# Kernel tuning notes

Measured on AMD Instinct MI355X. Metric: run time of the kernel, lower is better.

## Reference

```python
import jax, jax.numpy as jnp
import numpy as np

B, TQ, TK, D, NA = 8, 512, 2048, 1024, 512
H, HD = 16, 64          # n_head, head_dim (D = H*HD)
NE, HID = 4, 32         # n_experts, expert hidden_dim
EPS = 1e-6


def _rmsnorm(x, w):
    return x * jax.lax.rsqrt(jnp.mean(x * x, axis=-1, keepdims=True) + EPS) * w


def setup_inputs() -> dict:
    key = jax.random.key(0)
    ks = jax.random.split(key, 20)
    r = lambda i, shp: jax.random.normal(ks[i], shp, dtype=jnp.float32) * 0.02
    return {
        'q': jax.random.normal(ks[0], (B, TQ, D), dtype=jnp.float32),
        'kv': jax.random.normal(ks[1], (B, TK, D), dtype=jnp.float32),
        'qn_w': jnp.ones((D,), jnp.float32),
        'kva_w': jnp.ones((D,), jnp.float32),
        'kvi_w': jnp.ones((D,), jnp.float32),
        'dn_w': jnp.ones((D,), jnp.float32),
        'fn_w': jnp.ones((D,), jnp.float32),
        'Wq': r(2, (D, D)), 'bq': jnp.zeros((D,), jnp.float32),
        'Wk': r(3, (D, D)), 'bk': jnp.zeros((D,), jnp.float32),
        'Wv': r(4, (D, D)), 'bv': jnp.zeros((D,), jnp.float32),
        'Wo': r(5, (D, D)), 'bo': jnp.zeros((D,), jnp.float32),
        'active_bias': r(6, (D,)),
        'inactive_bias': r(7, (D,)),
        'log_temp': jnp.array(0.0, jnp.float32),
        'gate_attn': jnp.array(0.3, jnp.float32),
        'gate_ffn': jnp.array(0.7, jnp.float32),
        'Wr': r(8, (D, NE)), 'br': jnp.zeros((NE,), jnp.float32),
        'W1': r(9, (NE, D, 2 * HID)), 'b1': jnp.zeros((NE, 2 * HID), jnp.float32),
        'W2': r(10, (NE, HID, D)), 'b2': jnp.zeros((NE, D), jnp.float32),
        'kv_mask': jnp.ones((B, TK), bool),
        'n_actives': NA,
    }


def _forward(q, kv, qn_w, kva_w, kvi_w, dn_w, fn_w,
             Wq, bq, Wk, bk, Wv, bv, Wo, bo,
             active_bias, inactive_bias, log_temp, gate_attn, gate_ffn,
             Wr, br, W1, b1, W2, b2, kv_mask, n_actives):
    Na = int(n_actives)
    Tk = kv.shape[1]
    Ni = Tk - Na
    b, tq, d = q.shape

    # split-normed kv, with active/inactive learned biases injected pre-KV-proj
    kv_a = _rmsnorm(kv[:, :Na], kva_w) + active_bias
    kv_i = _rmsnorm(kv[:, Na:], kvi_w) + inactive_bias
    kv_b = jnp.concatenate([kv_a, kv_i], axis=1)

    qn = _rmsnorm(q, qn_w)
    qp = (qn @ Wq + bq).reshape(b, tq, H, HD).transpose(0, 2, 1, 3)  # (B,H,Tq,hd)
    k = (kv_b @ Wk + bk).reshape(b, Tk, H, HD).transpose(0, 2, 1, 3)
    v = (kv_b @ Wv + bv).reshape(b, Tk, H, HD).transpose(0, 2, 1, 3)

    # torch: q *= 1/sqrt(hd), then SDPA(q/temp, ...) applies another 1/sqrt(hd)
    temp = jnp.clip(jnp.exp(log_temp), 0.1, 10.0)
    scale = 1.0 / (HD * temp)

    def attn(kk, vv):
        logits = jnp.einsum('bhqd,bhkd->bhqk', qp, kk) * scale
        return jnp.einsum('bhqk,bhkd->bhqd', jax.nn.softmax(logits, axis=-1), vv)

    out = attn(k[:, :, :Na], v[:, :, :Na]) / np.sqrt(max(Na, 1)) \
        - attn(k[:, :, Na:], v[:, :, Na:]) / np.sqrt(max(Ni, 1))
    out = out.transpose(0, 2, 1, 3).reshape(b, tq, d)
    delta = _rmsnorm(out @ Wo + bo, dn_w)
    q_new = q + jax.nn.sigmoid(gate_attn) * delta

    # dense soft MoE over normed kv, with query-similarity logit bias
    x = _rmsnorm(kv, fn_w)
    logits = x @ Wr + br                                   # (B,Tk,NE)
    q_vec = jnp.mean(q_new, axis=1, keepdims=True)         # (B,1,D)
    sim = jnp.einsum('bqd,btd->bt', q_vec, x)              # (B,Tk)
    probs = jax.nn.softmax(logits + sim[..., None], axis=-1)

    h = jnp.einsum('btd,edh->bteh', x, W1) + b1            # (B,Tk,NE,2*HID)
    xp, g = h[..., :HID], h[..., HID:]
    act = xp * (g * jax.nn.sigmoid(g))                     # SwiGLU
    eo = jnp.einsum('bteh,ehd->bted', act, W2) + b2        # (B,Tk,NE,D)
    moe_out = jnp.einsum('bte,bted->btd', probs, eo)

    kv_new = kv + jax.nn.sigmoid(gate_ffn) * moe_out
    return q_new, kv_new


def reference(q, kv, qn_w, kva_w, kvi_w, dn_w, fn_w,
              Wq, bq, Wk, bk, Wv, bv, Wo, bo,
              active_bias, inactive_bias, log_temp, gate_attn, gate_ffn,
              Wr, br, W1, b1, W2, b2, kv_mask, n_actives):
    return _forward(q, kv, qn_w, kva_w, kvi_w, dn_w, fn_w,
                    Wq, bq, Wk, bk, Wv, bv, Wo, bo,
                    active_bias, inactive_bias, log_temp, gate_attn, gate_ffn,
                    Wr, br, W1, b1, W2, b2, kv_mask, n_actives)
```

## Files before the change

kernel.cpp:

```cpp
#include <hip/hip_runtime.h>
#include <hip/hip_bf16.h>
#include <stdint.h>


#define B_   8
#define TQ_  512
#define TK_  2048
#define D_   1024
#define H_   16
#define HD_  64
#define NE_  4
#define HID_ 32
#define EPSF 1e-6f
#define LOG2E 1.44269504f

typedef __bf16 bf16_t;
typedef __bf16 bf16x8 __attribute__((ext_vector_type(8)));
typedef __bf16 bf16x4 __attribute__((ext_vector_type(4)));
typedef float  f32x4  __attribute__((ext_vector_type(4)));

typedef __attribute__((address_space(1))) void gvoid_t;
typedef __attribute__((address_space(3))) void lvoid_t;

__device__ __forceinline__ void gld_lds16(const void* g, void* l) {
  __builtin_amdgcn_global_load_lds((gvoid_t*)g, (lvoid_t*)l, 16, 0, 0);
}

__global__ void transpose_conv_kernel(const float* __restrict__ in, bf16_t* __restrict__ out,
                                      int R, int C, int in_bstride,
                                      int out_rstride, int ob_row, int ob_col) {
  __shared__ float tile[32][33];
  const int bz = blockIdx.z;
  const int rb = blockIdx.y * 32, cb = blockIdx.x * 32;
  const int txi = threadIdx.x, tyi = threadIdx.y;
  const float* inp = in + (size_t)bz * in_bstride;
#pragma unroll
  for (int i = 0; i < 32; i += 8) {
    const int r = rb + tyi + i, c = cb + txi;
    if (r < R && c < C) tile[tyi + i][txi] = inp[(size_t)r * C + c];
  }
  __syncthreads();
#pragma unroll
  for (int i = 0; i < 32; i += 8) {
    const int orow = cb + tyi + i;
    const int ocol = rb + txi;
    if (orow < C && ocol < R)
      out[(size_t)(orow + bz * ob_row) * out_rstride + bz * ob_col + ocol] =
          (bf16_t)tile[txi][tyi + i];
  }
}

__device__ __forceinline__ float block_rsum(float v, float* red) {
  v += __shfl_xor(v, 1);  v += __shfl_xor(v, 2);  v += __shfl_xor(v, 4);
  v += __shfl_xor(v, 8);  v += __shfl_xor(v, 16); v += __shfl_xor(v, 32);
  const int tid = threadIdx.x;
  if ((tid & 63) == 0) red[tid >> 6] = v;
  __syncthreads();
  return red[0] + red[1] + red[2] + red[3];
}

__global__ __launch_bounds__(256)
void rms_kv_kernel(const float* __restrict__ kv, const float* __restrict__ kva_w,
                   const float* __restrict__ kvi_w, const float* __restrict__ fn_w,
                   const float* __restrict__ ab, const float* __restrict__ ib,
                   const int* __restrict__ n_act, const float* __restrict__ Wr,
                   const float* __restrict__ br,
                   bf16_t* __restrict__ kvb, bf16_t* __restrict__ xn,
                   float* __restrict__ probs) {
  __shared__ float red[4];
  __shared__ f32x4 pred[4];
  const int row = blockIdx.x;
  const int t = row & (TK_ - 1);
  const int tid = threadIdx.x;
  const float* src = kv + (size_t)row * D_;
  f32x4 v = ((const f32x4*)src)[tid];
  float ss = v[0]*v[0] + v[1]*v[1] + v[2]*v[2] + v[3]*v[3];
  ss = block_rsum(ss, red);
  const float rs = rsqrtf(ss * (1.0f / D_) + EPSF);
  const int Na = n_act[0];
  const float* wsel = (t < Na) ? kva_w : kvi_w;
  const float* bsel = (t < Na) ? ab : ib;
  const int d = tid * 4;
  f32x4 wv = *(const f32x4*)(wsel + d);
  f32x4 bv = *(const f32x4*)(bsel + d);
  f32x4 fv = *(const f32x4*)(fn_w + d);
  bf16x4 o0, o1;
  f32x4 p4 = {};
#pragma unroll
  for (int c = 0; c < 4; ++c) {
    const float xv = v[c] * rs;
    const float xf = xv * fv[c];
    o0[c] = (bf16_t)(xv * wv[c] + bv[c]);
    o1[c] = (bf16_t)xf;
    const f32x4 w4 = *(const f32x4*)&Wr[(d + c) * 4];
    p4 += w4 * xf;
  }
  *(bf16x4*)&kvb[(size_t)row * D_ + d] = o0;
  *(bf16x4*)&xn [(size_t)row * D_ + d] = o1;
#pragma unroll
  for (int m = 1; m <= 32; m <<= 1) {
    p4[0] += __shfl_xor(p4[0], m); p4[1] += __shfl_xor(p4[1], m);
    p4[2] += __shfl_xor(p4[2], m); p4[3] += __shfl_xor(p4[3], m);
  }
  if ((tid & 63) == 0) pred[tid >> 6] = p4;
  __syncthreads();
  if (tid == 0) {
    f32x4 s = pred[0] + pred[1] + pred[2] + pred[3];
    s[0] += br[0]; s[1] += br[1]; s[2] += br[2]; s[3] += br[3];
    const float mx = fmaxf(fmaxf(s[0], s[1]), fmaxf(s[2], s[3]));
    const float e0 = __expf(s[0] - mx), e1 = __expf(s[1] - mx);
    const float e2 = __expf(s[2] - mx), e3 = __expf(s[3] - mx);
    const float inv = 1.0f / (e0 + e1 + e2 + e3);
    f32x4 pr = { e0 * inv, e1 * inv, e2 * inv, e3 * inv };
    *(f32x4*)&probs[row * 4] = pr;
  }
}

__global__ __launch_bounds__(256)
void rms_q_kernel(const float* __restrict__ q, const float* __restrict__ qn_w,
                  bf16_t* __restrict__ qn) {
  __shared__ float red[4];
  const int row = blockIdx.x;
  const int tid = threadIdx.x;
  const float* src = q + (size_t)row * D_;
  f32x4 v = ((const f32x4*)src)[tid];
  float ss = v[0]*v[0] + v[1]*v[1] + v[2]*v[2] + v[3]*v[3];
  ss = block_rsum(ss, red);
  const float rs = rsqrtf(ss * (1.0f / D_) + EPSF);
  const int d = tid * 4;
  f32x4 wv = *(const f32x4*)(qn_w + d);
  bf16x4 o0;
#pragma unroll
  for (int c = 0; c < 4; ++c) o0[c] = (bf16_t)(v[c] * rs * wv[c]);
  *(bf16x4*)&qn[(size_t)row * D_ + d] = o0;
}

template<int HAS_BIAS>
__global__ __launch_bounds__(256)
void gemm_tn(const bf16_t* __restrict__ A, const bf16_t* __restrict__ Wt,
             const float* __restrict__ bias, bf16_t* __restrict__ C,
             int M, int N, int K) {
  __shared__ alignas(16) bf16_t As[128 * 32];
  __shared__ alignas(16) bf16_t Bs[128 * 32];
  const int tid = threadIdx.x;
  const int lane = tid & 63;
  const int w = tid >> 6;
  const int wr = w >> 1, wc = w & 1;
  const int m0 = blockIdx.x * 128;
  const int n0 = blockIdx.y * 128;

  f32x4 acc[4][4] = {};

  const int eidx = tid * 8;
  const int srow = eidx >> 5;
  const int scol = eidx & 31;
  const bf16_t* ga = A  + (size_t)(m0 + srow) * K + scol;
  const bf16_t* gb = Wt + (size_t)(n0 + srow) * K + scol;
  bf16_t* la0 = &As[tid * 8];
  bf16_t* la1 = &As[2048 + tid * 8];
  bf16_t* lb0 = &Bs[tid * 8];
  bf16_t* lb1 = &Bs[2048 + tid * 8];
  const size_t rstep = (size_t)64 * K;

  const int kb = (lane >> 4) * 8;
  const int ar  = (wr * 64 + (lane & 15)) * 32 + kb;
  const int br2 = (wc * 64 + (lane & 15)) * 32 + kb;

  for (int k0 = 0; k0 < K; k0 += 32) {
    gld_lds16(ga + k0,         la0);
    gld_lds16(ga + k0 + rstep, la1);
    gld_lds16(gb + k0,         lb0);
    gld_lds16(gb + k0 + rstep, lb1);
    __syncthreads();
    bf16x8 af[4], bfr[4];
#pragma unroll
    for (int i = 0; i < 4; ++i) af[i]  = *(const bf16x8*)&As[ar  + i * 512];
#pragma unroll
    for (int j = 0; j < 4; ++j) bfr[j] = *(const bf16x8*)&Bs[br2 + j * 512];
#pragma unroll
    for (int i = 0; i < 4; ++i)
#pragma unroll
      for (int j = 0; j < 4; ++j)
        acc[i][j] = __builtin_amdgcn_mfma_f32_16x16x32_bf16(af[i], bfr[j], acc[i][j], 0, 0, 0);
    __syncthreads();
  }

  const int row0 = m0 + wr * 64 + ((lane >> 4) << 2);
  const int col0 = n0 + wc * 64 + (lane & 15);
#pragma unroll
  for (int j = 0; j < 4; ++j) {
    const int cc = col0 + j * 16;
    const float bv = HAS_BIAS ? bias[cc] : 0.0f;
#pragma unroll
    for (int i = 0; i < 4; ++i) {
      const int rr = row0 + i * 16;
#pragma unroll
      for (int r = 0; r < 4; ++r)
        C[(size_t)(rr + r) * N + cc] = (bf16_t)(acc[i][j][r] + bv);
    }
  }
}

__global__ __launch_bounds__(256)
void gemm_vt(const bf16_t* __restrict__ A, const bf16_t* __restrict__ Wt0,
             const float* __restrict__ bias, bf16_t* __restrict__ C0) {
  __shared__ alignas(16) bf16_t As[128 * 32];
  __shared__ alignas(16) bf16_t Bs[128 * 32];
  const int K = D_, N = TK_;
  const bf16_t* Wt = Wt0 + (size_t)blockIdx.z * TK_ * D_;
  bf16_t* C = C0 + (size_t)blockIdx.z * D_ * TK_;
  const int tid = threadIdx.x;
  const int lane = tid & 63;
  const int w = tid >> 6;
  const int wr = w >> 1, wc = w & 1;
  const int m0 = blockIdx.x * 128;
  const int n0 = blockIdx.y * 128;

  f32x4 acc[4][4] = {};

  const int eidx = tid * 8;
  const int srow = eidx >> 5;
  const int scol = eidx & 31;
  const bf16_t* ga = A  + (size_t)(m0 + srow) * K + scol;
  const bf16_t* gb = Wt + (size_t)(n0 + srow) * K + scol;
  bf16_t* la0 = &As[tid * 8];
  bf16_t* la1 = &As[2048 + tid * 8];
  bf16_t* lb0 = &Bs[tid * 8];
  bf16_t* lb1 = &Bs[2048 + tid * 8];
  const size_t rstep = (size_t)64 * K;

  const int kb = (lane >> 4) * 8;
  const int ar  = (wr * 64 + (lane & 15)) * 32 + kb;
  const int br2 = (wc * 64 + (lane & 15)) * 32 + kb;

  for (int k0 = 0; k0 < K; k0 += 32) {
    gld_lds16(ga + k0,         la0);
    gld_lds16(ga + k0 + rstep, la1);
    gld_lds16(gb + k0,         lb0);
    gld_lds16(gb + k0 + rstep, lb1);
    __syncthreads();
    bf16x8 af[4], bfr[4];
#pragma unroll
    for (int i = 0; i < 4; ++i) af[i]  = *(const bf16x8*)&As[ar  + i * 512];
#pragma unroll
    for (int j = 0; j < 4; ++j) bfr[j] = *(const bf16x8*)&Bs[br2 + j * 512];
#pragma unroll
    for (int i = 0; i < 4; ++i)
#pragma unroll
      for (int j = 0; j < 4; ++j)
        acc[i][j] = __builtin_amdgcn_mfma_f32_16x16x32_bf16(af[i], bfr[j], acc[i][j], 0, 0, 0);
    __syncthreads();
  }

  const int row0 = m0 + wr * 64 + ((lane >> 4) << 2);
  const int col0 = n0 + wc * 64 + (lane & 15);
#pragma unroll
  for (int i = 0; i < 4; ++i) {
    const int rr = row0 + i * 16;
#pragma unroll
    for (int r = 0; r < 4; ++r) {
      const float bv = bias[rr + r];
#pragma unroll
      for (int j = 0; j < 4; ++j)
        C[(size_t)(rr + r) * N + col0 + j * 16] = (bf16_t)(acc[i][j][r] + bv);
    }
  }
}

__global__ __launch_bounds__(256)
void gemm_h_act(const bf16_t* __restrict__ A, const bf16_t* __restrict__ Wt,
                const float* __restrict__ bias, const float* __restrict__ probs,
                bf16_t* __restrict__ a2) {
  __shared__ alignas(16) bf16_t As[128 * 32];
  __shared__ alignas(16) bf16_t Bs[128 * 32];
  const int K = D_;
  const int tid = threadIdx.x;
  const int lane = tid & 63;
  const int w = tid >> 6;
  const int wr = w >> 1, wc = w & 1;
  const int m0 = blockIdx.x * 128;
  const int n0 = blockIdx.y * 128;

  f32x4 acc[4][4] = {};

  const int eidx = tid * 8;
  const int srow = eidx >> 5;
  const int scol = eidx & 31;
  const bf16_t* ga = A  + (size_t)(m0 + srow) * K + scol;
  const bf16_t* gb = Wt + (size_t)(n0 + srow) * K + scol;
  bf16_t* la0 = &As[tid * 8];
  bf16_t* la1 = &As[2048 + tid * 8];
  bf16_t* lb0 = &Bs[tid * 8];
  bf16_t* lb1 = &Bs[2048 + tid * 8];
  const size_t rstep = (size_t)64 * K;

  const int kb = (lane >> 4) * 8;
  const int ar  = (wr * 64 + (lane & 15)) * 32 + kb;
  const int br2 = (wc * 64 + (lane & 15)) * 32 + kb;

  for (int k0 = 0; k0 < K; k0 += 32) {
    gld_lds16(ga + k0,         la0);
    gld_lds16(ga + k0 + rstep, la1);
    gld_lds16(gb + k0,         lb0);
    gld_lds16(gb + k0 + rstep, lb1);
    __syncthreads();
    bf16x8 af[4], bfr[4];
#pragma unroll
    for (int i = 0; i < 4; ++i) af[i]  = *(const bf16x8*)&As[ar  + i * 512];
#pragma unroll
    for (int j = 0; j < 4; ++j) bfr[j] = *(const bf16x8*)&Bs[br2 + j * 512];
#pragma unroll
    for (int i = 0; i < 4; ++i)
#pragma unroll
      for (int j = 0; j < 4; ++j)
        acc[i][j] = __builtin_amdgcn_mfma_f32_16x16x32_bf16(af[i], bfr[j], acc[i][j], 0, 0, 0);
    __syncthreads();
  }

  const int row0 = m0 + wr * 64 + ((lane >> 4) << 2);
  const int hbase = n0 + wc * 64 + (lane & 15);
  const int e = hbase >> 6;
#pragma unroll
  for (int j = 0; j < 2; ++j) {
    const int ch = hbase + j * 16;
    const float bx = bias[ch], bg = bias[ch + 32];
    const int ac = (ch & 63) + e * 32;
#pragma unroll
    for (int i = 0; i < 4; ++i) {
      const int rr = row0 + i * 16;
#pragma unroll
      for (int r = 0; r < 4; ++r) {
        const float xp = acc[i][j][r] + bx;
        const float g  = acc[i][j + 2][r] + bg;
        const float sg = 1.0f / (1.0f + __expf(-g));
        const float pr = probs[(size_t)(rr + r) * 4 + e];
        a2[(size_t)(rr + r) * 128 + ac] = (bf16_t)(pr * xp * g * sg);
      }
    }
  }
}

__global__ __launch_bounds__(256)
void gemm_moe_kvnew(const bf16_t* __restrict__ A, const bf16_t* __restrict__ Wt,
                    const float* __restrict__ kv, const float* __restrict__ probs,
                    const float* __restrict__ b2, const float* __restrict__ gate_ffn,
                    float* __restrict__ out) {
  __shared__ alignas(16) bf16_t As[128 * 32];
  __shared__ alignas(16) bf16_t Bs[128 * 32];
  const int K = 128, N = D_;
  const int tid = threadIdx.x;
  const int lane = tid & 63;
  const int w = tid >> 6;
  const int wr = w >> 1, wc = w & 1;
  const int m0 = blockIdx.x * 128;
  const int n0 = blockIdx.y * 128;

  f32x4 acc[4][4] = {};

  const int eidx = tid * 8;
  const int srow = eidx >> 5;
  const int scol = eidx & 31;
  const bf16_t* ga = A  + (size_t)(m0 + srow) * K + scol;
  const bf16_t* gb = Wt + (size_t)(n0 + srow) * K + scol;
  bf16_t* la0 = &As[tid * 8];
  bf16_t* la1 = &As[2048 + tid * 8];
  bf16_t* lb0 = &Bs[tid * 8];
  bf16_t* lb1 = &Bs[2048 + tid * 8];
  const size_t rstep = (size_t)64 * K;

  const int kb = (lane >> 4) * 8;
  const int ar  = (wr * 64 + (lane & 15)) * 32 + kb;
  const int br2 = (wc * 64 + (lane & 15)) * 32 + kb;

  for (int k0 = 0; k0 < K; k0 += 32) {
    gld_lds16(ga + k0,         la0);
    gld_lds16(ga + k0 + rstep, la1);
    gld_lds16(gb + k0,         lb0);
    gld_lds16(gb + k0 + rstep, lb1);
    __syncthreads();
    bf16x8 af[4], bfr[4];
#pragma unroll
    for (int i = 0; i < 4; ++i) af[i]  = *(const bf16x8*)&As[ar  + i * 512];
#pragma unroll
    for (int j = 0; j < 4; ++j) bfr[j] = *(const bf16x8*)&Bs[br2 + j * 512];
#pragma unroll
    for (int i = 0; i < 4; ++i)
#pragma unroll
      for (int j = 0; j < 4; ++j)
        acc[i][j] = __builtin_amdgcn_mfma_f32_16x16x32_bf16(af[i], bfr[j], acc[i][j], 0, 0, 0);
    __syncthreads();
  }

  const float sgf = 1.0f / (1.0f + __expf(-gate_ffn[0]));
  const int row0 = m0 + wr * 64 + ((lane >> 4) << 2);
  const int col0 = n0 + wc * 64 + (lane & 15);
#pragma unroll
  for (int j = 0; j < 4; ++j) {
    const int cc = col0 + j * 16;
    const f32x4 b2v = { b2[0 * D_ + cc], b2[1 * D_ + cc], b2[2 * D_ + cc], b2[3 * D_ + cc] };
#pragma unroll
    for (int i = 0; i < 4; ++i) {
      const int rr = row0 + i * 16;
#pragma unroll
      for (int r = 0; r < 4; ++r) {
        const f32x4 pr = *(const f32x4*)&probs[(size_t)(rr + r) * 4];
        const float bsum = pr[0]*b2v[0] + pr[1]*b2v[1] + pr[2]*b2v[2] + pr[3]*b2v[3];
        out[(size_t)(rr + r) * N + cc] =
            kv[(size_t)(rr + r) * N + cc] + sgf * (acc[i][j][r] + bsum);
      }
    }
  }
}

__global__ __launch_bounds__(512, 2)
void attn_mfma_kernel(const bf16_t* __restrict__ qp, const bf16_t* __restrict__ kb,
                      const bf16_t* __restrict__ vt, bf16_t* __restrict__ attno,
                      const float* __restrict__ log_temp, const int* __restrict__ n_act) {
  __shared__ alignas(16) bf16_t Ks[2][64 * 64];
  __shared__ alignas(16) bf16_t Vs[2][64 * 64];
  __shared__ alignas(16) bf16_t Ps[8][16 * 64];

  const int dd = blockIdx.x;
  const int xcd = dd & 7, within = dd >> 3;
  const int qt = within & 3, slot = within >> 2;
  const int bh = slot * 8 + xcd;
  const int b = bh >> 4, h = bh & 15;

  const int tid = threadIdx.x;
  const int lane = tid & 63;
  const int w = tid >> 6;
  const int lane15 = lane & 15, lgrp = lane >> 4, l7 = lane & 7;
  const int Na = n_act[0];
  float temp = __expf(log_temp[0]);
  temp = fminf(fmaxf(temp, 0.1f), 10.0f);
  const float lsc = LOG2E / (64.0f * temp);
  const int q0 = qt * 128;

  const bf16_t* qsrc = qp + (size_t)(b * TQ_ + q0 + w * 16 + lane15) * D_ + h * 64 + lgrp * 8;
  const bf16x8 qf0 = *(const bf16x8*)qsrc;
  const bf16x8 qf1 = *(const bf16x8*)(qsrc + 32);

  const int srow = tid >> 3;
  const int schunk = (tid & 7) ^ (srow & 7);
  const bf16_t* ksrc = kb + (size_t)(b * TK_ + srow) * D_ + h * 64 + schunk * 8;
  const bf16_t* vsrc = vt + ((size_t)(b * 16 + h) * 64 + srow) * TK_ + schunk * 8;

  f32x4 o[4] = {};
  f32x4 outa[4] = {};
  f32x4 lacc = {};

  const float inv_sa = rsqrtf((float)(Na > 1 ? Na : 1));
  const int Ni = TK_ - Na;
  const float inv_si = rsqrtf((float)(Ni > 1 ? Ni : 1));

  gld_lds16(ksrc, &Ks[0][tid * 8]);
  gld_lds16(vsrc, &Vs[0][tid * 8]);

  for (int t = 0; t < TK_ / 64; ++t) {
    const int cur = t & 1;
    __syncthreads();
    if (t + 1 < TK_ / 64) {
      const int nb = cur ^ 1;
      gld_lds16(ksrc + (size_t)(t + 1) * 64 * D_, &Ks[nb][tid * 8]);
      gld_lds16(vsrc + (size_t)(t + 1) * 64,      &Vs[nb][tid * 8]);
    }

    f32x4 sacc[4];
#pragma unroll
    for (int cf = 0; cf < 4; ++cf) {
      const int krow = (cf * 16 + lane15) * 64;
      const bf16x8 kf0 = *(const bf16x8*)&Ks[cur][krow + ((lgrp ^ l7) << 3)];
      const bf16x8 kf1 = *(const bf16x8*)&Ks[cur][krow + (((lgrp + 4) ^ l7) << 3)];
      f32x4 s = {};
      s = __builtin_amdgcn_mfma_f32_16x16x32_bf16(qf0, kf0, s, 0, 0, 0);
      s = __builtin_amdgcn_mfma_f32_16x16x32_bf16(qf1, kf1, s, 0, 0, 0);
      sacc[cf] = s;
    }

#pragma unroll
    for (int cf = 0; cf < 4; ++cf) {
      const int kp = cf * 16 + lane15;
      const int kcb = kp >> 3, kin = kp & 7;
      f32x4 p;
#pragma unroll
      for (int r = 0; r < 4; ++r) p[r] = exp2f(sacc[cf][r] * lsc);
      lacc += p;
#pragma unroll
      for (int r = 0; r < 4; ++r) {
        const int ql = lgrp * 4 + r;
        Ps[w][ql * 64 + ((kcb ^ (ql & 7)) << 3) + kin] = (bf16_t)p[r];
      }
    }

    {
      const int prow = lane15 * 64;
      const bf16x8 pa0 = *(const bf16x8*)&Ps[w][prow + ((lgrp ^ l7) << 3)];
      const bf16x8 pa1 = *(const bf16x8*)&Ps[w][prow + (((lgrp + 4) ^ l7) << 3)];
#pragma unroll
      for (int df = 0; df < 4; ++df) {
        const int vrow = (df * 16 + lane15) * 64;
        const bf16x8 vf0 = *(const bf16x8*)&Vs[cur][vrow + ((lgrp ^ l7) << 3)];
        const bf16x8 vf1 = *(const bf16x8*)&Vs[cur][vrow + (((lgrp + 4) ^ l7) << 3)];
        o[df] = __builtin_amdgcn_mfma_f32_16x16x32_bf16(pa0, vf0, o[df], 0, 0, 0);
        o[df] = __builtin_amdgcn_mfma_f32_16x16x32_bf16(pa1, vf1, o[df], 0, 0, 0);
      }
    }

    const bool endA = ((t + 1) * 64 == Na);
    const bool endI = (t == TK_ / 64 - 1);
    if (endA || endI) {
      const float ssc = endA ? inv_sa : -inv_si;
      f32x4 rl = lacc;
#pragma unroll
      for (int r = 0; r < 4; ++r) {
        rl[r] += __shfl_xor(rl[r], 1);
        rl[r] += __shfl_xor(rl[r], 2);
        rl[r] += __shfl_xor(rl[r], 4);
        rl[r] += __shfl_xor(rl[r], 8);
      }
      f32x4 iv;
#pragma unroll
      for (int r = 0; r < 4; ++r) iv[r] = ssc / rl[r];
#pragma unroll
      for (int df = 0; df < 4; ++df) { outa[df] += o[df] * iv; o[df] = (f32x4){}; }
      lacc = (f32x4){};
    }
  }

#pragma unroll
  for (int df = 0; df < 4; ++df)
#pragma unroll
    for (int r = 0; r < 4; ++r)
      attno[(size_t)(b * TQ_ + q0 + w * 16 + lgrp * 4 + r) * D_ + h * 64 + df * 16 + lane15] =
          (bf16_t)outa[df][r];
}

__global__ __launch_bounds__(256)
void delta_qnew_kernel(const bf16_t* __restrict__ proj, const float* __restrict__ dn_w,
                       const float* __restrict__ q, const float* __restrict__ gate_attn,
                       float* __restrict__ qnew) {
  __shared__ float red[4];
  const int row = blockIdx.x;
  const int tid = threadIdx.x;
  bf16x4 pv = *(const bf16x4*)(proj + (size_t)row * D_ + tid * 4);
  f32x4 v;
#pragma unroll
  for (int c = 0; c < 4; ++c) v[c] = (float)pv[c];
  float ss = v[0]*v[0] + v[1]*v[1] + v[2]*v[2] + v[3]*v[3];
  ss = block_rsum(ss, red);
  const float rs = rsqrtf(ss * (1.0f / D_) + EPSF);
  const float sga = 1.0f / (1.0f + __expf(-gate_attn[0]));
  const int d = tid * 4;
  f32x4 wv = *(const f32x4*)(dn_w + d);
  f32x4 qv = *(const f32x4*)(q + (size_t)row * D_ + d);
  f32x4 out;
#pragma unroll
  for (int c = 0; c < 4; ++c) out[c] = qv[c] + sga * (v[c] * rs * wv[c]);
  *(f32x4*)&qnew[(size_t)row * D_ + d] = out;
}

extern "C" void kernel_launch(void* const* d_in, const int* in_sizes, int n_in,
                              void* d_out, int out_size, void* d_ws, size_t ws_size,
                              hipStream_t stream) {
  const float* q           = (const float*)d_in[0];
  const float* kv          = (const float*)d_in[1];
  const float* qn_w        = (const float*)d_in[2];
  const float* kva_w       = (const float*)d_in[3];
  const float* kvi_w       = (const float*)d_in[4];
  const float* dn_w        = (const float*)d_in[5];
  const float* fn_w        = (const float*)d_in[6];
  const float* Wq          = (const float*)d_in[7];
  const float* bq          = (const float*)d_in[8];
  const float* Wk          = (const float*)d_in[9];
  const float* bk          = (const float*)d_in[10];
  const float* Wv          = (const float*)d_in[11];
  const float* bv          = (const float*)d_in[12];
  const float* Wo          = (const float*)d_in[13];
  const float* bo          = (const float*)d_in[14];
  const float* active_bias = (const float*)d_in[15];
  const float* inactive_b  = (const float*)d_in[16];
  const float* log_temp    = (const float*)d_in[17];
  const float* gate_attn   = (const float*)d_in[18];
  const float* gate_ffn    = (const float*)d_in[19];
  const float* Wr          = (const float*)d_in[20];
  const float* br          = (const float*)d_in[21];
  const float* W1          = (const float*)d_in[22];
  const float* b1          = (const float*)d_in[23];
  const float* W2          = (const float*)d_in[24];
  const float* b2          = (const float*)d_in[25];
  const int*   n_act       = (const int*)d_in[27];

  char* ws = (char*)d_ws;
  size_t off = 0;
  auto alloc = [&](size_t bytes) -> char* {
    char* p = ws + off;
    off = (off + bytes + 255) & ~(size_t)255;
    return p;
  };

  bf16_t* wqT  = (bf16_t*)alloc((size_t)D_ * D_ * 2);
  bf16_t* wkT  = (bf16_t*)alloc((size_t)D_ * D_ * 2);
  bf16_t* wvT  = (bf16_t*)alloc((size_t)D_ * D_ * 2);
  bf16_t* woT  = (bf16_t*)alloc((size_t)D_ * D_ * 2);
  bf16_t* w1T  = (bf16_t*)alloc((size_t)256 * D_ * 2);
  bf16_t* w2T  = (bf16_t*)alloc((size_t)D_ * 128 * 2);
  bf16_t* kvb  = (bf16_t*)alloc((size_t)B_ * TK_ * D_ * 2);
  bf16_t* xn   = (bf16_t*)alloc((size_t)B_ * TK_ * D_ * 2);
  bf16_t* qn   = (bf16_t*)alloc((size_t)B_ * TQ_ * D_ * 2);
  bf16_t* qp   = (bf16_t*)alloc((size_t)B_ * TQ_ * D_ * 2);
  bf16_t* kbuf = (bf16_t*)alloc((size_t)B_ * TK_ * D_ * 2);
  bf16_t* vt   = (bf16_t*)alloc((size_t)B_ * D_ * TK_ * 2);
  float*  probs = (float*)alloc((size_t)B_ * TK_ * NE_ * 4);
  bf16_t* attno = qn;
  bf16_t* proj  = qp;
  bf16_t* a2buf = kbuf;
  (void)ws_size; (void)in_sizes; (void)n_in; (void)out_size;

  float* q_new_out  = (float*)d_out;
  float* kv_new_out = (float*)d_out + (size_t)B_ * TQ_ * D_;

  dim3 tb(32, 8);
  transpose_conv_kernel<<<dim3(32, 32, 1), tb, 0, stream>>>(Wq, wqT, D_, D_, 0, D_, 0, 0);
  transpose_conv_kernel<<<dim3(32, 32, 1), tb, 0, stream>>>(Wk, wkT, D_, D_, 0, D_, 0, 0);
  transpose_conv_kernel<<<dim3(32, 32, 1), tb, 0, stream>>>(Wv, wvT, D_, D_, 0, D_, 0, 0);
  transpose_conv_kernel<<<dim3(32, 32, 1), tb, 0, stream>>>(Wo, woT, D_, D_, 0, D_, 0, 0);
  transpose_conv_kernel<<<dim3(2, 32, 4), tb, 0, stream>>>(W1, w1T, D_, 64, D_ * 64, D_, 64, 0);
  transpose_conv_kernel<<<dim3(32, 1, 4), tb, 0, stream>>>(W2, w2T, 32, D_, 32 * D_, 128, 0, 32);

  rms_kv_kernel<<<B_ * TK_, 256, 0, stream>>>(kv, kva_w, kvi_w, fn_w, active_bias,
                                              inactive_b, n_act, Wr, br, kvb, xn, probs);
  rms_q_kernel<<<B_ * TQ_, 256, 0, stream>>>(q, qn_w, qn);

  gemm_tn<1><<<dim3(B_ * TQ_ / 128, D_ / 128), 256, 0, stream>>>(qn, wqT, bq, qp, B_ * TQ_, D_, D_);
  gemm_tn<1><<<dim3(B_ * TK_ / 128, D_ / 128), 256, 0, stream>>>(kvb, wkT, bk, kbuf, B_ * TK_, D_, D_);
  gemm_vt<<<dim3(D_ / 128, TK_ / 128, B_), 256, 0, stream>>>(wvT, kvb, bv, vt);

  attn_mfma_kernel<<<B_ * H_ * (TQ_ / 128), 512, 0, stream>>>(qp, kbuf, vt, attno, log_temp, n_act);

  gemm_tn<1><<<dim3(B_ * TQ_ / 128, D_ / 128), 256, 0, stream>>>(attno, woT, bo, proj, B_ * TQ_, D_, D_);
  delta_qnew_kernel<<<B_ * TQ_, 256, 0, stream>>>(proj, dn_w, q, gate_attn, q_new_out);

  gemm_h_act<<<dim3(B_ * TK_ / 128, 2), 256, 0, stream>>>(xn, w1T, b1, probs, a2buf);
  gemm_moe_kvnew<<<dim3(B_ * TK_ / 128, D_ / 128), 256, 0, stream>>>(a2buf, w2T, kv, probs, b2,
                                                                     gate_ffn, kv_new_out);
}
```

Before: 368.3 us.

## Double-buffer GEMM LDS loads, swizzle blocks across XCDs, transpose attention score MFMA

New measurement: 357.3 us. -3.0%, faster.

```diff
diff --git a/kernel.cpp b/kernel.cpp
--- a/kernel.cpp
+++ b/kernel.cpp
@@ -135,13 +135,94 @@
   *(bf16x4*)&qn[(size_t)row * D_ + d] = o0;
 }
 
+__device__ __forceinline__ void gemm_loop_db(const bf16_t* __restrict__ ga,
+                                             const bf16_t* __restrict__ gb,
+                                             bf16_t* As, bf16_t* Bs, int K,
+                                             size_t rstep, int ar, int br2,
+                                             int tid, f32x4 acc[4][4]) {
+  gld_lds16(ga,         &As[tid * 8]);
+  gld_lds16(ga + rstep, &As[2048 + tid * 8]);
+  gld_lds16(gb,         &Bs[tid * 8]);
+  gld_lds16(gb + rstep, &Bs[2048 + tid * 8]);
+  int buf = 0;
+  for (int k0 = 0; k0 < K; k0 += 32) {
+    __syncthreads();
+    if (k0 + 32 < K) {
+      const int nb = buf ^ 1;
+      gld_lds16(ga + k0 + 32,         &As[nb * 4096 + tid * 8]);
+      gld_lds16(ga + k0 + 32 + rstep, &As[nb * 4096 + 2048 + tid * 8]);
+      gld_lds16(gb + k0 + 32,         &Bs[nb * 4096 + tid * 8]);
+      gld_lds16(gb + k0 + 32 + rstep, &Bs[nb * 4096 + 2048 + tid * 8]);
+    }
+    bf16x8 af[4], bfr[4];
+#pragma unroll
+    for (int i = 0; i < 4; ++i) af[i]  = *(const bf16x8*)&As[buf * 4096 + ar  + i * 512];
+#pragma unroll
+    for (int j = 0; j < 4; ++j) bfr[j] = *(const bf16x8*)&Bs[buf * 4096 + br2 + j * 512];
+#pragma unroll
+    for (int i = 0; i < 4; ++i)
+#pragma unroll
+      for (int j = 0; j < 4; ++j)
+        acc[i][j] = __builtin_amdgcn_mfma_f32_16x16x32_bf16(af[i], bfr[j], acc[i][j], 0, 0, 0);
+    buf ^= 1;
+  }
+}
+
+__device__ __forceinline__ int xcd_swz(int bx, int gx) {
+  if ((gx & 7) == 0) { const int cpx = gx >> 3; return (bx & 7) * cpx + (bx >> 3); }
+  return bx;
+}
+
 template<int HAS_BIAS>
 __global__ __launch_bounds__(256)
 void gemm_tn(const bf16_t* __restrict__ A, const bf16_t* __restrict__ Wt,
              const float* __restrict__ bias, bf16_t* __restrict__ C,
              int M, int N, int K) {
-  __shared__ alignas(16) bf16_t As[128 * 32];
-  __shared__ alignas(16) bf16_t Bs[128 * 32];
+  __shared__ alignas(16) bf16_t As[2 * 128 * 32];
+  __shared__ alignas(16) bf16_t Bs[2 * 128 * 32];
+  const int tid = threadIdx.x;
+  const int lane = tid & 63;
+  const int w = tid >> 6;
+  const int wr = w >> 1, wc = w & 1;
+  const int m0 = xcd_swz(blockIdx.x, gridDim.x) * 128;
+  const int n0 = blockIdx.y * 128;
+
+  f32x4 acc[4][4] = {};
+  const int eidx = tid * 8;
+  const int srow = eidx >> 5;
+  const int scol = eidx & 31;
+  const bf16_t* ga = A  + (size_t)(m0 + srow) * K + scol;
+  const bf16_t* gb = Wt + (size_t)(n0 + srow) * K + scol;
+  const int kb = (lane >> 4) * 8;
+  const int ar  = (wr * 64 + (lane & 15)) * 32 + kb;
+  const int br2 = (wc * 64 + (lane & 15)) * 32 + kb;
+
+  gemm_loop_db(ga, gb, As, Bs, K, (size_t)64 * K, ar, br2, tid, acc);
+
+  const int row0 = m0 + wr * 64 + ((lane >> 4) << 2);
+  const int col0 = n0 + wc * 64 + (lane & 15);
+#pragma unroll
+  for (int j = 0; j < 4; ++j) {
+    const int cc = col0 + j * 16;
+    const float bv = HAS_BIAS ? bias[cc] : 0.0f;
+#pragma unroll
+    for (int i = 0; i < 4; ++i) {
+      const int rr = row0 + i * 16;
+#pragma unroll
+      for (int r = 0; r < 4; ++r)
+        C[(size_t)(rr + r) * N + cc] = (bf16_t)(acc[i][j][r] + bv);
+    }
+  }
+}
+
+__global__ __launch_bounds__(256)
+void gemm_vt(const bf16_t* __restrict__ A, const bf16_t* __restrict__ Wt0,
+             const float* __restrict__ bias, bf16_t* __restrict__ C0) {
+  __shared__ alignas(16) bf16_t As[2 * 128 * 32];
+  __shared__ alignas(16) bf16_t Bs[2 * 128 * 32];
+  const int K = D_, N = TK_;
+  const bf16_t* Wt = Wt0 + (size_t)blockIdx.z * TK_ * D_;
+  bf16_t* C = C0 + (size_t)blockIdx.z * D_ * TK_;
   const int tid = threadIdx.x;
   const int lane = tid & 63;
   const int w = tid >> 6;
@@ -150,172 +231,57 @@
   const int n0 = blockIdx.y * 128;
 
   f32x4 acc[4][4] = {};
-
   const int eidx = tid * 8;
   const int srow = eidx >> 5;
   const int scol = eidx & 31;
   const bf16_t* ga = A  + (size_t)(m0 + srow) * K + scol;
   const bf16_t* gb = Wt + (size_t)(n0 + srow) * K + scol;
-  bf16_t* la0 = &As[tid * 8];
-  bf16_t* la1 = &As[2048 + tid * 8];
-  bf16_t* lb0 = &Bs[tid * 8];
-  bf16_t* lb1 = &Bs[2048 + tid * 8];
-  const size_t rstep = (size_t)64 * K;
-
   const int kb = (lane >> 4) * 8;
   const int ar  = (wr * 64 + (lane & 15)) * 32 + kb;
   const int br2 = (wc * 64 + (lane & 15)) * 32 + kb;
 
-  for (int k0 = 0; k0 < K; k0 += 32) {
-    gld_lds16(ga + k0,         la0);
-    gld_lds16(ga + k0 + rstep, la1);
-    gld_lds16(gb + k0,         lb0);
-    gld_lds16(gb + k0 + rstep, lb1);
-    __syncthreads();
-    bf16x8 af[4], bfr[4];
-#pragma unroll
-    for (int i = 0; i < 4; ++i) af[i]  = *(const bf16x8*)&As[ar  + i * 512];
-#pragma unroll
-    for (int j = 0; j < 4; ++j) bfr[j] = *(const bf16x8*)&Bs[br2 + j * 512];
-#pragma unroll
-    for (int i = 0; i < 4; ++i)
-#pragma unroll
-      for (int j = 0; j < 4; ++j)
-        acc[i][j] = __builtin_amdgcn_mfma_f32_16x16x32_bf16(af[i], bfr[j], acc[i][j], 0, 0, 0);
-    __syncthreads();
-  }
+  gemm_loop_db(ga, gb, As, Bs, K, (size_t)64 * K, ar, br2, tid, acc);
 
   const int row0 = m0 + wr * 64 + ((lane >> 4) << 2);
   const int col0 = n0 + wc * 64 + (lane & 15);
 #pragma unroll
-  for (int j = 0; j < 4; ++j) {
-    const int cc = col0 + j * 16;
-    const float bv = HAS_BIAS ? bias[cc] : 0.0f;
-#pragma unroll
-    for (int i = 0; i < 4; ++i) {
-      const int rr = row0 + i * 16;
-#pragma unroll
-      for (int r = 0; r < 4; ++r)
-        C[(size_t)(rr + r) * N + cc] = (bf16_t)(acc[i][j][r] + bv);
-    }
-  }
-}
-
-__global__ __launch_bounds__(256)
-void gemm_vt(const bf16_t* __restrict__ A, const bf16_t* __restrict__ Wt0,
-             const float* __restrict__ bias, bf16_t* __restrict__ C0) {
-  __shared__ alignas(16) bf16_t As[128 * 32];
-  __shared__ alignas(16) bf16_t Bs[128 * 32];
-  const int K = D_, N = TK_;
-  const bf16_t* Wt = Wt0 + (size_t)blockIdx.z * TK_ * D_;
-  bf16_t* C = C0 + (size_t)blockIdx.z * D_ * TK_;
+  for (int i = 0; i < 4; ++i) {
+    const int rr = row0 + i * 16;
+#pragma unroll
+    for (int r = 0; r < 4; ++r) {
+      const float bv = bias[rr + r];
+#pragma unroll
+      for (int j = 0; j < 4; ++j)
+        C[(size_t)(rr + r) * N + col0 + j * 16] = (bf16_t)(acc[i][j][r] + bv);
+    }
+  }
+}
+
+__global__ __launch_bounds__(256)
+void gemm_h_act(const bf16_t* __restrict__ A, const bf16_t* __restrict__ Wt,
+                const float* __restrict__ bias, const float* __restrict__ probs,
+                bf16_t* __restrict__ a2) {
+  __shared__ alignas(16) bf16_t As[2 * 128 * 32];
+  __shared__ alignas(16) bf16_t Bs[2 * 128 * 32];
+  const int K = D_;
   const int tid = threadIdx.x;
   const int lane = tid & 63;
   const int w = tid >> 6;
   const int wr = w >> 1, wc = w & 1;
-  const int m0 = blockIdx.x * 128;
+  const int m0 = xcd_swz(blockIdx.x, gridDim.x) * 128;
   const int n0 = blockIdx.y * 128;
 
   f32x4 acc[4][4] = {};
-
   const int eidx = tid * 8;
   const int srow = eidx >> 5;
   const int scol = eidx & 31;
   const bf16_t* ga = A  + (size_t)(m0 + srow) * K + scol;
   const bf16_t* gb = Wt + (size_t)(n0 + srow) * K + scol;
-  bf16_t* la0 = &As[tid * 8];
-  bf16_t* la1 = &As[2048 + tid * 8];
-  bf16_t* lb0 = &Bs[tid * 8];
-  bf16_t* lb1 = &Bs[2048 + tid * 8];
-  const size_t rstep = (size_t)64 * K;
-
   const int kb = (lane >> 4) * 8;
   const int ar  = (wr * 64 + (lane & 15)) * 32 + kb;
   const int br2 = (wc * 64 + (lane & 15)) * 32 + kb;
 
-  for (int k0 = 0; k0 < K; k0 += 32) {
-    gld_lds16(ga + k0,         la0);
-    gld_lds16(ga + k0 + rstep, la1);
-    gld_lds16(gb + k0,         lb0);
-    gld_lds16(gb + k0 + rstep, lb1);
-    __syncthreads();
-    bf16x8 af[4], bfr[4];
-#pragma unroll
-    for (int i = 0; i < 4; ++i) af[i]  = *(const bf16x8*)&As[ar  + i * 512];
-#pragma unroll
-    for (int j = 0; j < 4; ++j) bfr[j] = *(const bf16x8*)&Bs[br2 + j * 512];
-#pragma unroll
-    for (int i = 0; i < 4; ++i)
-#pragma unroll
-      for (int j = 0; j < 4; ++j)
-        acc[i][j] = __builtin_amdgcn_mfma_f32_16x16x32_bf16(af[i], bfr[j], acc[i][j], 0, 0, 0);
-    __syncthreads();
-  }
-
-  const int row0 = m0 + wr * 64 + ((lane >> 4) << 2);
-  const int col0 = n0 + wc * 64 + (lane & 15);
-#pragma unroll
-  for (int i = 0; i < 4; ++i) {
-    const int rr = row0 + i * 16;
-#pragma unroll
-    for (int r = 0; r < 4; ++r) {
-      const float bv = bias[rr + r];
-#pragma unroll
-      for (int j = 0; j < 4; ++j)
-        C[(size_t)(rr + r) * N + col0 + j * 16] = (bf16_t)(acc[i][j][r] + bv);
-    }
-  }
-}
-
-__global__ __launch_bounds__(256)
-void gemm_h_act(const bf16_t* __restrict__ A, const bf16_t* __restrict__ Wt,
-                const float* __restrict__ bias, const float* __restrict__ probs,
-                bf16_t* __restrict__ a2) {
-  __shared__ alignas(16) bf16_t As[128 * 32];
-  __shared__ alignas(16) bf16_t Bs[128 * 32];
-  const int K = D_;
-  const int tid = threadIdx.x;
-  const int lane = tid & 63;
-  const int w = tid >> 6;
-  const int wr = w >> 1, wc = w & 1;
-  const int m0 = blockIdx.x * 128;
-  const int n0 = blockIdx.y * 128;
-
-  f32x4 acc[4][4] = {};
-
-  const int eidx = tid * 8;
-  const int srow = eidx >> 5;
-  const int scol = eidx & 31;
-  const bf16_t* ga = A  + (size_t)(m0 + srow) * K + scol;
-  const bf16_t* gb = Wt + (size_t)(n0 + srow) * K + scol;
-  bf16_t* la0 = &As[tid * 8];
-  bf16_t* la1 = &As[2048 + tid * 8];
-  bf16_t* lb0 = &Bs[tid * 8];
-  bf16_t* lb1 = &Bs[2048 + tid * 8];
-  const size_t rstep = (size_t)64 * K;
-
-  const int kb = (lane >> 4) * 8;
-  const int ar  = (wr * 64 + (lane & 15)) * 32 + kb;
-  const int br2 = (wc * 64 + (lane & 15)) * 32 + kb;
-
-  for (int k0 = 0; k0 < K; k0 += 32) {
-    gld_lds16(ga + k0,         la0);
-    gld_lds16(ga + k0 + rstep, la1);
-    gld_lds16(gb + k0,         lb0);
-    gld_lds16(gb + k0 + rstep, lb1);
-    __syncthreads();
-    bf16x8 af[4], bfr[4];
-#pragma unroll
-    for (int i = 0; i < 4; ++i) af[i]  = *(const bf16x8*)&As[ar  + i * 512];
-#pragma unroll
-    for (int j = 0; j < 4; ++j) bfr[j] = *(const bf16x8*)&Bs[br2 + j * 512];
-#pragma unroll
-    for (int i = 0; i < 4; ++i)
-#pragma unroll
-      for (int j = 0; j < 4; ++j)
-        acc[i][j] = __builtin_amdgcn_mfma_f32_16x16x32_bf16(af[i], bfr[j], acc[i][j], 0, 0, 0);
-    __syncthreads();
-  }
+  gemm_loop_db(ga, gb, As, Bs, K, (size_t)64 * K, ar, br2, tid, acc);
 
   const int row0 = m0 + wr * 64 + ((lane >> 4) << 2);
   const int hbase = n0 + wc * 64 + (lane & 15);
@@ -345,51 +311,27 @@
                     const float* __restrict__ kv, const float* __restrict__ probs,
                     const float* __restrict__ b2, const float* __restrict__ gate_ffn,
                     float* __restrict__ out) {
-  __shared__ alignas(16) bf16_t As[128 * 32];
-  __shared__ alignas(16) bf16_t Bs[128 * 32];
+  __shared__ alignas(16) bf16_t As[2 * 128 * 32];
+  __shared__ alignas(16) bf16_t Bs[2 * 128 * 32];
   const int K = 128, N = D_;
   const int tid = threadIdx.x;
   const int lane = tid & 63;
   const int w = tid >> 6;
   const int wr = w >> 1, wc = w & 1;
-  const int m0 = blockIdx.x * 128;
+  const int m0 = xcd_swz(blockIdx.x, gridDim.x) * 128;
   const int n0 = blockIdx.y * 128;
 
   f32x4 acc[4][4] = {};
-
   const int eidx = tid * 8;
   const int srow = eidx >> 5;
   const int scol = eidx & 31;
   const bf16_t* ga = A  + (size_t)(m0 + srow) * K + scol;
   const bf16_t* gb = Wt + (size_t)(n0 + srow) * K + scol;
-  bf16_t* la0 = &As[tid * 8];
-  bf16_t* la1 = &As[2048 + tid * 8];
-  bf16_t* lb0 = &Bs[tid * 8];
-  bf16_t* lb1 = &Bs[2048 + tid * 8];
-  const size_t rstep = (size_t)64 * K;
-
   const int kb = (lane >> 4) * 8;
   const int ar  = (wr * 64 + (lane & 15)) * 32 + kb;
   const int br2 = (wc * 64 + (lane & 15)) * 32 + kb;
 
-  for (int k0 = 0; k0 < K; k0 += 32) {
-    gld_lds16(ga + k0,         la0);
-    gld_lds16(ga + k0 + rstep, la1);
-    gld_lds16(gb + k0,         lb0);
-    gld_lds16(gb + k0 + rstep, lb1);
-    __syncthreads();
-    bf16x8 af[4], bfr[4];
-#pragma unroll
-    for (int i = 0; i < 4; ++i) af[i]  = *(const bf16x8*)&As[ar  + i * 512];
-#pragma unroll
-    for (int j = 0; j < 4; ++j) bfr[j] = *(const bf16x8*)&Bs[br2 + j * 512];
-#pragma unroll
-    for (int i = 0; i < 4; ++i)
-#pragma unroll
-      for (int j = 0; j < 4; ++j)
-        acc[i][j] = __builtin_amdgcn_mfma_f32_16x16x32_bf16(af[i], bfr[j], acc[i][j], 0, 0, 0);
-    __syncthreads();
-  }
+  gemm_loop_db(ga, gb, As, Bs, K, (size_t)64 * K, ar, br2, tid, acc);
 
   const float sgf = 1.0f / (1.0f + __expf(-gate_ffn[0]));
   const int row0 = m0 + wr * 64 + ((lane >> 4) << 2);
@@ -422,8 +364,8 @@
 
   const int dd = blockIdx.x;
   const int xcd = dd & 7, within = dd >> 3;
-  const int qt = within & 3, slot = within >> 2;
-  const int bh = slot * 8 + xcd;
+  const int qt = within & 3, slot0 = within >> 2;
+  const int bh = slot0 * 8 + xcd;
   const int b = bh >> 4, h = bh & 15;
 
   const int tid = threadIdx.x;
@@ -437,8 +379,13 @@
   const int q0 = qt * 128;
 
   const bf16_t* qsrc = qp + (size_t)(b * TQ_ + q0 + w * 16 + lane15) * D_ + h * 64 + lgrp * 8;
-  const bf16x8 qf0 = *(const bf16x8*)qsrc;
-  const bf16x8 qf1 = *(const bf16x8*)(qsrc + 32);
+  bf16x8 qf0 = *(const bf16x8*)qsrc;
+  bf16x8 qf1 = *(const bf16x8*)(qsrc + 32);
+#pragma unroll
+  for (int j = 0; j < 8; ++j) {
+    qf0[j] = (bf16_t)((float)qf0[j] * lsc);
+    qf1[j] = (bf16_t)((float)qf1[j] * lsc);
+  }
 
   const int srow = tid >> 3;
   const int schunk = (tid & 7) ^ (srow & 7);
@@ -447,7 +394,7 @@
 
   f32x4 o[4] = {};
   f32x4 outa[4] = {};
-  f32x4 lacc = {};
+  float lacc = 0.f;
 
   const float inv_sa = rsqrtf((float)(Na > 1 ? Na : 1));
   const int Ni = TK_ - Na;
@@ -472,24 +419,22 @@
       const bf16x8 kf0 = *(const bf16x8*)&Ks[cur][krow + ((lgrp ^ l7) << 3)];
       const bf16x8 kf1 = *(const bf16x8*)&Ks[cur][krow + (((lgrp + 4) ^ l7) << 3)];
       f32x4 s = {};
-      s = __builtin_amdgcn_mfma_f32_16x16x32_bf16(qf0, kf0, s, 0, 0, 0);
-      s = __builtin_amdgcn_mfma_f32_16x16x32_bf16(qf1, kf1, s, 0, 0, 0);
+      s = __builtin_amdgcn_mfma_f32_16x16x32_bf16(kf0, qf0, s, 0, 0, 0);
+      s = __builtin_amdgcn_mfma_f32_16x16x32_bf16(kf1, qf1, s, 0, 0, 0);
       sacc[cf] = s;
     }
 
 #pragma unroll
     for (int cf = 0; cf < 4; ++cf) {
-      const int kp = cf * 16 + lane15;
-      const int kcb = kp >> 3, kin = kp & 7;
       f32x4 p;
 #pragma unroll
-      for (int r = 0; r < 4; ++r) p[r] = exp2f(sacc[cf][r] * lsc);
-      lacc += p;
-#pragma unroll
-      for (int r = 0; r < 4; ++r) {
-        const int ql = lgrp * 4 + r;
-        Ps[w][ql * 64 + ((kcb ^ (ql & 7)) << 3) + kin] = (bf16_t)p[r];
-      }
+      for (int r = 0; r < 4; ++r) p[r] = exp2f(sacc[cf][r]);
+      lacc += (p[0] + p[1]) + (p[2] + p[3]);
+      bf16x4 pv4;
+#pragma unroll
+      for (int r = 0; r < 4; ++r) pv4[r] = (bf16_t)p[r];
+      const int c = cf * 2 + (lgrp >> 1);
+      *(bf16x4*)&Ps[w][lane15 * 64 + ((c ^ l7) << 3) + (lgrp & 1) * 4] = pv4;
     }
 
     {
@@ -509,21 +454,16 @@
     const bool endA = ((t + 1) * 64 == Na);
     const bool endI = (t == TK_ / 64 - 1);
     if (endA || endI) {
+      float l = lacc;
+      l += __shfl_xor(l, 16);
+      l += __shfl_xor(l, 32);
       const float ssc = endA ? inv_sa : -inv_si;
-      f32x4 rl = lacc;
-#pragma unroll
-      for (int r = 0; r < 4; ++r) {
-        rl[r] += __shfl_xor(rl[r], 1);
-        rl[r] += __shfl_xor(rl[r], 2);
-        rl[r] += __shfl_xor(rl[r], 4);
-        rl[r] += __shfl_xor(rl[r], 8);
-      }
       f32x4 iv;
 #pragma unroll
-      for (int r = 0; r < 4; ++r) iv[r] = ssc / rl[r];
+      for (int r = 0; r < 4; ++r) iv[r] = ssc / __shfl(l, lgrp * 4 + r);
 #pragma unroll
       for (int df = 0; df < 4; ++df) { outa[df] += o[df] * iv; o[df] = (f32x4){}; }
-      lacc = (f32x4){};
+      lacc = 0.f;
     }
   }
 
```
